# Kernel tuning notes

Hardware: AMD Instinct MI355X
Metric: run time of the kernel (lower is better)

Reference implementation:

```python
import jax, jax.numpy as jnp
import numpy as np

CONF_TH = 0.9
FRACTION = 0.66
IGNORE_INDEX = 255
LAMBDA = 1.0


def setup_inputs() -> dict:
    key = jax.random.key(0)
    pred = jax.random.normal(key, (4, 19, 512, 1024), dtype=jnp.float32)
    return {"pred": pred}


def _image_mask(max_prob, pseudo, num_classes):
    # max_prob, pseudo: [N] flattened per-image. Replicates the torch per-class
    # loop: keep the top floor(count_c * FRACTION) pixels of each class c by
    # max_prob. Equivalent to: within-class descending rank < k_c.
    n = max_prob.shape[0]
    # sort by (class asc, prob desc); last key in lexsort is primary
    order = jnp.lexsort((-max_prob, pseudo))
    counts = jnp.bincount(pseudo, length=num_classes)  # [C]
    starts = jnp.concatenate([jnp.zeros(1, counts.dtype), jnp.cumsum(counts)[:-1]])
    rank_sorted = jnp.arange(n, dtype=counts.dtype) - starts[pseudo[order]]
    rank = jnp.zeros(n, counts.dtype).at[order].set(rank_sorted)
    k = jnp.floor(counts.astype(jnp.float32) * FRACTION).astype(counts.dtype)  # int(count*frac)
    mask_topk = rank < k[pseudo]
    mask_prob = max_prob > CONF_TH
    return mask_prob | mask_topk


def reference(pred):
    B, C, H, W = pred.shape
    logp = jax.nn.log_softmax(pred, axis=1)           # [B,C,H,W]
    prob = jnp.exp(logp)
    pseudo = jnp.argmax(pred, axis=1)                 # [B,H,W] (detached in torch; int here)
    max_prob = jnp.max(prob, axis=1)                  # [B,H,W]
    N = H * W
    mask = jax.vmap(lambda m, p: _image_mask(m, p, C))(
        max_prob.reshape(B, N), pseudo.reshape(B, N)
    ).reshape(B, H, W)
    target = jnp.where(mask, pseudo, IGNORE_INDEX)
    valid = target != IGNORE_INDEX
    tsafe = jnp.where(valid, target, 0)
    nll = -jnp.take_along_axis(logp, tsafe[:, None], axis=1)[:, 0]  # [B,H,W]
    # F.cross_entropy(..., reduction='none') gives 0 at ignored pixels; .mean()
    # divides by the TOTAL number of pixels (including ignored ones).
    loss = jnp.where(valid, nll, 0.0).mean() * LAMBDA
    return loss
```

## Files before the change

### kernel.cpp

```cpp
#include <hip/hip_runtime.h>
#include <math.h>

#define BB 4
#define CC 19
#define HH 512
#define WW 1024
#define NPIX (HH * WW)
#define NB 80
#define CONF_BIN 72
#define FRACTION_F 0.66f
#define ROW (CC * NB)
#define NROW (BB * CC)

#define NBLK1 512
#define BPI (NBLK1 / BB)
#define PPB (NPIX / BPI)
#define T1 512


static __device__ __forceinline__ float comp(float4 v, int j) {
    return (j == 0) ? v.x : (j == 1) ? v.y : (j == 2) ? v.z : v.w;
}

__global__ __launch_bounds__(T1, 4) void st_pass1(const float* __restrict__ pred,
                                                  int* __restrict__ cntPart,
                                                  float* __restrict__ snlPart) {
    __shared__ int   hcnt[ROW];
    __shared__ float hsnl[ROW];
    int tid = threadIdx.x;
    for (int i = tid; i < ROW; i += T1) { hcnt[i] = 0; hsnl[i] = 0.f; }
    __syncthreads();

    int blk = blockIdx.x;
    int b   = blk >> 7;
    int seg = blk & (BPI - 1);
    const float* base = pred + (size_t)b * CC * NPIX + (size_t)seg * PPB;

    #pragma unroll
    for (int it = 0; it < 2; ++it) {
        const float* bp = base + it * (T1 * 4) + tid * 4;
        float4 v0[5], v1[5], v2[5], v3[4];

        #pragma unroll
        for (int i = 0; i < 5; ++i) v0[i] = *(const float4*)(bp + (size_t)i * NPIX);
        #pragma unroll
        for (int i = 0; i < 5; ++i) v1[i] = *(const float4*)(bp + (size_t)(5 + i) * NPIX);
        asm volatile("" ::: "memory");

        float m[4], s[4]; int arg[4];
        #pragma unroll
        for (int j = 0; j < 4; ++j) { m[j] = comp(v0[0], j); s[j] = 1.f; arg[j] = 0; }

#define PROC(VA, NCH, CBASE, START)                                   \
        _Pragma("unroll")                                             \
        for (int i = START; i < NCH; ++i) {                           \
            _Pragma("unroll")                                         \
            for (int j = 0; j < 4; ++j) {                             \
                float x  = comp(VA[i], j);                            \
                float nm = fmaxf(m[j], x);                            \
                s[j] = s[j] * __expf(m[j] - nm) + __expf(x - nm);     \
                arg[j] = (x > m[j]) ? (CBASE + i) : arg[j];           \
                m[j] = nm;                                            \
            }                                                         \
        }

        PROC(v0, 5, 0, 1)
        #pragma unroll
        for (int i = 0; i < 5; ++i) v2[i] = *(const float4*)(bp + (size_t)(10 + i) * NPIX);
        asm volatile("" ::: "memory");
        PROC(v1, 5, 5, 0)
        #pragma unroll
        for (int i = 0; i < 4; ++i) v3[i] = *(const float4*)(bp + (size_t)(15 + i) * NPIX);
        asm volatile("" ::: "memory");
        PROC(v2, 5, 10, 0)
        PROC(v3, 4, 15, 0)
#undef PROC

        #pragma unroll
        for (int j = 0; j < 4; ++j) {
            float prob = 1.f / s[j];
            float nll  = __logf(s[j]);
            int bin = (int)(prob * (float)NB);
            bin = min(bin, NB - 1);
            int idx = arg[j] * NB + bin;
            atomicAdd(&hcnt[idx], 1);
            atomicAdd(&hsnl[idx], nll);
        }
    }
    __syncthreads();

    int*   cp = cntPart + (size_t)blk * ROW;
    float* sp = snlPart + (size_t)blk * ROW;
    for (int i = tid; i < ROW; i += T1) { cp[i] = hcnt[i]; sp[i] = hsnl[i]; }
}

__global__ __launch_bounds__(128) void st_pass2(const int* __restrict__ cntPart,
                                                const float* __restrict__ snlPart,
                                                float* __restrict__ selbuf) {
    __shared__ int   scnt[NB];
    __shared__ float ssnl[NB];
    int r = blockIdx.x;
    int b = r / CC, c = r - b * CC;
    int tid = threadIdx.x;

    if (tid < NB) {
        size_t off = (size_t)(b * BPI) * ROW + (size_t)(c * NB + tid);
        int cs0 = 0, cs1 = 0; float ss0 = 0.f, ss1 = 0.f;
        #pragma unroll 8
        for (int p = 0; p < BPI; p += 2) {
            cs0 += cntPart[off + (size_t)p * ROW];
            cs1 += cntPart[off + (size_t)(p + 1) * ROW];
            ss0 += snlPart[off + (size_t)p * ROW];
            ss1 += snlPart[off + (size_t)(p + 1) * ROW];
        }
        scnt[tid] = cs0 + cs1;
        ssnl[tid] = ss0 + ss1;
    }
    __syncthreads();

    if (tid == 0) {
        int count = 0;
        #pragma unroll 8
        for (int i = 0; i < NB; ++i) count += scnt[i];
        float conf = 0.f;
        #pragma unroll 8
        for (int i = CONF_BIN; i < NB; ++i) conf += ssnl[i];
        int k = (int)floorf((float)count * FRACTION_F);
        float sel;
        if (k == 0) {
            sel = conf;
        } else {
            int cum = 0;
            float csum = 0.f;
            int bin = NB - 1;
            int hh = 0;
            for (; bin >= 0; --bin) {
                hh = scnt[bin];
                if (cum + hh >= k) break;
                cum += hh;
                csum += ssnl[bin];
            }
            if (bin < 0) {
                sel = csum;
            } else if (bin >= CONF_BIN) {
                sel = conf;
            } else {
                float avg = ssnl[bin] / (float)max(hh, 1);
                sel = csum + (float)(k - cum) * avg;
            }
        }
        selbuf[r] = sel;
    }
}

__global__ __launch_bounds__(128) void st_pass3(const float* __restrict__ selbuf,
                                                float* __restrict__ out) {
    __shared__ float red[128];
    int t = threadIdx.x;
    red[t] = (t < NROW) ? selbuf[t] : 0.f;
    __syncthreads();
    for (int off = 64; off > 0; off >>= 1) {
        if (t < off) red[t] += red[t + off];
        __syncthreads();
    }
    if (t == 0) out[0] = red[0] * (1.0f / (float)(BB * (size_t)NPIX));
}

extern "C" void kernel_launch(void* const* d_in, const int* in_sizes, int n_in,
                              void* d_out, int out_size, void* d_ws, size_t ws_size,
                              hipStream_t stream) {
    const float* pred = (const float*)d_in[0];
    float* out = (float*)d_out;

    char* ws = (char*)d_ws;
    int*   cntPart = (int*)ws;
    float* snlPart = (float*)(ws + (size_t)NBLK1 * ROW * sizeof(int));
    float* selbuf  = (float*)(ws + (size_t)NBLK1 * ROW * (sizeof(int) + sizeof(float)));

    st_pass1<<<NBLK1, T1, 0, stream>>>(pred, cntPart, snlPart);
    st_pass2<<<NROW, 128, 0, stream>>>(cntPart, snlPart, selbuf);
    st_pass3<<<1, 128, 0, stream>>>(selbuf, out);
}
```

Before: 45.80 us.

## Pipeline loads across pixel chunks, split pass2 reduction, fuse final sum via atomics

Pass1 now streams the second pixel chunk's loads while the first chunk's last channels are still being processed, using four rotating register buffers. Pass2 spreads the per-bin partial sums over four thread groups and then combines them. The final reduction kernel is removed: pass2 adds its scaled result straight into the output with an atomic, and pass1 zeroes the output first. This saves one kernel launch and exposes more memory-level parallelism, but the float atomic makes the summation order nondeterministic.

After: 41.63 us. 9.1% less time.

```diff
diff --git a/kernel.cpp b/kernel.cpp
--- a/kernel.cpp
+++ b/kernel.cpp
@@ -24,33 +24,36 @@
 
 __global__ __launch_bounds__(T1, 4) void st_pass1(const float* __restrict__ pred,
                                                   int* __restrict__ cntPart,
-                                                  float* __restrict__ snlPart) {
+                                                  float* __restrict__ snlPart,
+                                                  float* __restrict__ out) {
     __shared__ int   hcnt[ROW];
     __shared__ float hsnl[ROW];
     int tid = threadIdx.x;
+    if (blockIdx.x == 0 && tid == 0) out[0] = 0.f;
     for (int i = tid; i < ROW; i += T1) { hcnt[i] = 0; hsnl[i] = 0.f; }
     __syncthreads();
 
     int blk = blockIdx.x;
     int b   = blk >> 7;
     int seg = blk & (BPI - 1);
-    const float* base = pred + (size_t)b * CC * NPIX + (size_t)seg * PPB;
+    const float* bp0 = pred + (size_t)b * CC * NPIX + (size_t)seg * PPB + tid * 4;
+    const float* bp1 = bp0 + T1 * 4;
 
-    #pragma unroll
-    for (int it = 0; it < 2; ++it) {
-        const float* bp = base + it * (T1 * 4) + tid * 4;
-        float4 v0[5], v1[5], v2[5], v3[4];
+    float4 va[5], vb[5], vc[5], vd[4];
+    float m[4], s[4]; int arg[4];
 
-        #pragma unroll
-        for (int i = 0; i < 5; ++i) v0[i] = *(const float4*)(bp + (size_t)i * NPIX);
-        #pragma unroll
-        for (int i = 0; i < 5; ++i) v1[i] = *(const float4*)(bp + (size_t)(5 + i) * NPIX);
-        asm volatile("" ::: "memory");
-
-        float m[4], s[4]; int arg[4];
-        #pragma unroll
-        for (int j = 0; j < 4; ++j) { m[j] = comp(v0[0], j); s[j] = 1.f; arg[j] = 0; }
-
+#define LOAD5(DST, BP, C0)                                            \
+        _Pragma("unroll")                                             \
+        for (int i = 0; i < 5; ++i)                                   \
+            DST[i] = *(const float4*)((BP) + (size_t)(C0 + i) * NPIX);
+#define LOAD4(DST, BP, C0)                                            \
+        _Pragma("unroll")                                             \
+        for (int i = 0; i < 4; ++i)                                   \
+            DST[i] = *(const float4*)((BP) + (size_t)(C0 + i) * NPIX);
+#define FENCE asm volatile("" ::: "memory")
+#define INIT4(VA)                                                     \
+        _Pragma("unroll")                                             \
+        for (int j = 0; j < 4; ++j) { m[j] = comp(VA[0], j); s[j] = 1.f; arg[j] = 0; }
 #define PROC(VA, NCH, CBASE, START)                                   \
         _Pragma("unroll")                                             \
         for (int i = START; i < NCH; ++i) {                           \
@@ -63,30 +66,42 @@
                 m[j] = nm;                                            \
             }                                                         \
         }
+#define FINAL()                                                       \
+        _Pragma("unroll")                                             \
+        for (int j = 0; j < 4; ++j) {                                 \
+            float prob = 1.f / s[j];                                  \
+            float nll  = __logf(s[j]);                                \
+            int bin = min((int)(prob * (float)NB), NB - 1);           \
+            int idx = arg[j] * NB + bin;                              \
+            atomicAdd(&hcnt[idx], 1);                                 \
+            atomicAdd(&hsnl[idx], nll);                               \
+        }
 
-        PROC(v0, 5, 0, 1)
-        #pragma unroll
-        for (int i = 0; i < 5; ++i) v2[i] = *(const float4*)(bp + (size_t)(10 + i) * NPIX);
-        asm volatile("" ::: "memory");
-        PROC(v1, 5, 5, 0)
-        #pragma unroll
-        for (int i = 0; i < 4; ++i) v3[i] = *(const float4*)(bp + (size_t)(15 + i) * NPIX);
-        asm volatile("" ::: "memory");
-        PROC(v2, 5, 10, 0)
-        PROC(v3, 4, 15, 0)
+    LOAD5(va, bp0, 0); LOAD5(vb, bp0, 5); FENCE;
+    INIT4(va)
+    PROC(va, 5, 0, 1)
+    LOAD5(vc, bp0, 10); FENCE;
+    PROC(vb, 5, 5, 0)
+    LOAD4(vd, bp0, 15); FENCE;
+    PROC(vc, 5, 10, 0)
+    LOAD5(va, bp1, 0); FENCE;
+    PROC(vd, 4, 15, 0)
+    FINAL()
+    LOAD5(vb, bp1, 5); FENCE;
+    INIT4(va)
+    PROC(va, 5, 0, 1)
+    LOAD5(vc, bp1, 10); FENCE;
+    PROC(vb, 5, 5, 0)
+    LOAD4(vd, bp1, 15); FENCE;
+    PROC(vc, 5, 10, 0)
+    PROC(vd, 4, 15, 0)
+    FINAL()
+#undef LOAD5
+#undef LOAD4
+#undef FENCE
+#undef INIT4
 #undef PROC
-
-        #pragma unroll
-        for (int j = 0; j < 4; ++j) {
-            float prob = 1.f / s[j];
-            float nll  = __logf(s[j]);
-            int bin = (int)(prob * (float)NB);
-            bin = min(bin, NB - 1);
-            int idx = arg[j] * NB + bin;
-            atomicAdd(&hcnt[idx], 1);
-            atomicAdd(&hsnl[idx], nll);
-        }
-    }
+#undef FINAL
     __syncthreads();
 
     int*   cp = cntPart + (size_t)blk * ROW;
@@ -94,27 +109,36 @@
     for (int i = tid; i < ROW; i += T1) { cp[i] = hcnt[i]; sp[i] = hsnl[i]; }
 }
 
-__global__ __launch_bounds__(128) void st_pass2(const int* __restrict__ cntPart,
+__global__ __launch_bounds__(384) void st_pass2(const int* __restrict__ cntPart,
                                                 const float* __restrict__ snlPart,
-                                                float* __restrict__ selbuf) {
+                                                float* __restrict__ out) {
+    __shared__ int   pcnt[4][NB];
+    __shared__ float psnl[4][NB];
     __shared__ int   scnt[NB];
     __shared__ float ssnl[NB];
     int r = blockIdx.x;
     int b = r / CC, c = r - b * CC;
     int tid = threadIdx.x;
 
-    if (tid < NB) {
-        size_t off = (size_t)(b * BPI) * ROW + (size_t)(c * NB + tid);
+    if (tid < 4 * NB) {
+        int q   = tid / NB;
+        int bin = tid - q * NB;
+        size_t off = (size_t)(b * BPI + q * 32) * ROW + (size_t)(c * NB + bin);
         int cs0 = 0, cs1 = 0; float ss0 = 0.f, ss1 = 0.f;
         #pragma unroll 8
-        for (int p = 0; p < BPI; p += 2) {
+        for (int p = 0; p < 32; p += 2) {
             cs0 += cntPart[off + (size_t)p * ROW];
             cs1 += cntPart[off + (size_t)(p + 1) * ROW];
             ss0 += snlPart[off + (size_t)p * ROW];
             ss1 += snlPart[off + (size_t)(p + 1) * ROW];
         }
-        scnt[tid] = cs0 + cs1;
-        ssnl[tid] = ss0 + ss1;
+        pcnt[q][bin] = cs0 + cs1;
+        psnl[q][bin] = ss0 + ss1;
+    }
+    __syncthreads();
+    if (tid < NB) {
+        scnt[tid] = (pcnt[0][tid] + pcnt[1][tid]) + (pcnt[2][tid] + pcnt[3][tid]);
+        ssnl[tid] = (psnl[0][tid] + psnl[1][tid]) + (psnl[2][tid] + psnl[3][tid]);
     }
     __syncthreads();
 
@@ -149,21 +173,8 @@
                 sel = csum + (float)(k - cum) * avg;
             }
         }
-        selbuf[r] = sel;
+        atomicAdd(out, sel * (1.0f / (float)(BB * (size_t)NPIX)));
     }
-}
-
-__global__ __launch_bounds__(128) void st_pass3(const float* __restrict__ selbuf,
-                                                float* __restrict__ out) {
-    __shared__ float red[128];
-    int t = threadIdx.x;
-    red[t] = (t < NROW) ? selbuf[t] : 0.f;
-    __syncthreads();
-    for (int off = 64; off > 0; off >>= 1) {
-        if (t < off) red[t] += red[t + off];
-        __syncthreads();
-    }
-    if (t == 0) out[0] = red[0] * (1.0f / (float)(BB * (size_t)NPIX));
 }
 
 extern "C" void kernel_launch(void* const* d_in, const int* in_sizes, int n_in,
@@ -175,9 +186,7 @@
     char* ws = (char*)d_ws;
     int*   cntPart = (int*)ws;
     float* snlPart = (float*)(ws + (size_t)NBLK1 * ROW * sizeof(int));
-    float* selbuf  = (float*)(ws + (size_t)NBLK1 * ROW * (sizeof(int) + sizeof(float)));
 
-    st_pass1<<<NBLK1, T1, 0, stream>>>(pred, cntPart, snlPart);
-    st_pass2<<<NROW, 128, 0, stream>>>(cntPart, snlPart, selbuf);
-    st_pass3<<<1, 128, 0, stream>>>(selbuf, out);
+    st_pass1<<<NBLK1, T1, 0, stream>>>(pred, cntPart, snlPart, out);
+    st_pass2<<<NROW, 384, 0, stream>>>(cntPart, snlPart, out);
 }
```
